# Kernel tuning notes

Measured on AMD Instinct MI355X. Metric: run time of the kernel, lower is better.

Reference implementation:

```python
import jax, jax.numpy as jnp
import numpy as np

# Architecture constants from Dense_test.__init__
N_HID = 200      # n
BRANCH = 8
IN_DIM = 120     # 40 * 3
N_OUT = 12
VTH = 1.0        # vth=1, dt=1 -> R*dt factor = 1

# Multi-gaussian surrogate-gradient spike (ActFun_adp from DH-SNN)
LENS, SCALE, HIGHT, GAMMA = 0.5, 6.0, 0.15, 0.5

@jax.custom_vjp
def spike_fn(v):
    return (v > 0).astype(v.dtype)

def _spike_fwd(v):
    return (v > 0).astype(v.dtype), v

def _gauss(x, mu, sigma):
    return jnp.exp(-((x - mu) ** 2) / (2.0 * sigma ** 2)) / (jnp.sqrt(2.0 * jnp.pi) * sigma)

def _spike_bwd(v, g):
    sg = (_gauss(v, 0.0, LENS) * (1.0 + HIGHT)
          - _gauss(v, LENS, SCALE * LENS) * HIGHT
          - _gauss(v, -LENS, SCALE * LENS) * HIGHT)
    return (g * sg * GAMMA,)

spike_fn.defvjp(_spike_fwd, _spike_bwd)


def make_branch_mask(rng, in_features, out_dim, branch):
    # Each output neuron's dendritic branches connect to disjoint random
    # subsets of (input + recurrent) lines.
    k = in_features // branch
    mask = np.zeros((out_dim * branch, in_features), np.float32)
    for i in range(out_dim):
        seq = rng.permutation(in_features)
        for j in range(branch):
            mask[i * branch + j, seq[j * k:(j + 1) * k]] = 1.0
    return jnp.asarray(mask)


def setup_inputs() -> dict:
    rng = np.random.default_rng(0)
    key = jax.random.key(0)
    ks = jax.random.split(key, 16)
    B, T = 1024, 101
    d = {"x": jax.random.normal(ks[0], (B, 3, T, 40), jnp.float32)}
    in_feats = [IN_DIM + N_HID, N_HID + N_HID, N_HID + N_HID]
    for li, in_f in enumerate(in_feats, start=1):
        mask = make_branch_mask(rng, in_f, N_HID, BRANCH)
        W = jax.random.normal(ks[li], (N_HID * BRANCH, in_f), jnp.float32) / np.sqrt(in_f)
        d[f"W{li}"] = W * mask   # mask is applied multiplicatively to dense weights
        d[f"b{li}"] = jnp.zeros((N_HID * BRANCH,), jnp.float32)
        d[f"tau_m{li}"] = jax.random.uniform(ks[li + 4], (N_HID,), jnp.float32, 0.0, 4.0)
        d[f"tau_n{li}"] = jax.random.uniform(ks[li + 8], (N_HID, BRANCH), jnp.float32, 0.0, 4.0)
    d["W4"] = jax.random.normal(ks[12], (N_OUT, N_HID), jnp.float32) / np.sqrt(N_HID)
    d["b4"] = jnp.zeros((N_OUT,), jnp.float32)
    d["tau_m4"] = jax.random.uniform(ks[13], (N_OUT,), jnp.float32, 0.0, 4.0)
    return d


def _forward(x, W1, b1, tau_m1, tau_n1, W2, b2, tau_m2, tau_n2,
             W3, b3, tau_m3, tau_n3, W4, b4, tau_m4):
    B, C, T, F = x.shape
    xs = jnp.transpose(x, (2, 0, 1, 3)).reshape(T, B, C * F)  # [T, B, 120]

    def dense_step(inp, spike, d, mem, W, b, tau_m, tau_n):
        k = jnp.concatenate([inp, spike], axis=1)              # recurrent concat
        ff = (k @ W.T + b).reshape(B, N_HID, BRANCH)
        beta = jax.nn.sigmoid(tau_n)                           # [N_HID, BRANCH]
        d = beta * d + (1.0 - beta) * ff                       # dendritic current
        alpha = jax.nn.sigmoid(tau_m)
        mem = (mem - VTH * spike) * alpha + (1.0 - alpha) * d.sum(-1)
        spike = spike_fn(mem - VTH)
        return spike, d, mem

    z = lambda *s: jnp.zeros(s, x.dtype)
    init = (z(B, N_HID), z(B, N_HID, BRANCH), z(B, N_HID),
            z(B, N_HID), z(B, N_HID, BRANCH), z(B, N_HID),
            z(B, N_HID), z(B, N_HID, BRANCH), z(B, N_HID),
            z(B, N_OUT), z(B, N_OUT))
    alpha4 = jax.nn.sigmoid(tau_m4)

    def step(carry, xt):
        s1, d1, m1, s2, d2, m2, s3, d3, m3, m4, acc = carry
        s1, d1, m1 = dense_step(xt, s1, d1, m1, W1, b1, tau_m1, tau_n1)
        s2, d2, m2 = dense_step(s1, s2, d2, m2, W2, b2, tau_m2, tau_n2)
        s3, d3, m3 = dense_step(s2, s3, d3, m3, W3, b3, tau_m3, tau_n3)
        m4 = m4 * alpha4 + (1.0 - alpha4) * (s3 @ W4.T + b4)   # leaky readout
        acc = acc + m4
        return (s1, d1, m1, s2, d2, m2, s3, d3, m3, m4, acc), None

    carry, _ = jax.lax.scan(step, init, xs)
    acc = carry[-1]
    return jax.nn.log_softmax(acc / T, axis=1)


def reference(x, W1, b1, tau_m1, tau_n1, W2, b2, tau_m2, tau_n2,
              W3, b3, tau_m3, tau_n3, W4, b4, tau_m4):
    return _forward(x, W1, b1, tau_m1, tau_n1, W2, b2, tau_m2, tau_n2,
                    W3, b3, tau_m3, tau_n3, W4, b4, tau_m4)
```

## Files before the change

### kernel.cpp

```cpp
#include <hip/hip_runtime.h>
#include <stdint.h>

#define T_STEPS 101
#define ROWS 1600
#define NTHR 1024
#define NBLK 256
#define NP1 20
#define NP23 25
#define PO2 (NP1 * ROWS)
#define PO3 (PO2 + NP23 * ROWS)
#define NPTOT (PO3 + NP23 * ROWS)

#define W2_OFF 0
#define C2_OFF (NPTOT * 8)
#define BB_OFF (C2_OFF + NPTOT * 4)
#define SA_OFF (BB_OFF + 3 * ROWS * 8)

__device__ __forceinline__ float sigmoidf(float v) { return 1.0f / (1.0f + expf(-v)); }

__global__ void prep_kernel(const float* __restrict__ W1, const float* __restrict__ W2,
                            const float* __restrict__ W3,
                            const float* __restrict__ b1, const float* __restrict__ tn1,
                            const float* __restrict__ tm1,
                            const float* __restrict__ b2, const float* __restrict__ tn2,
                            const float* __restrict__ tm2,
                            const float* __restrict__ b3, const float* __restrict__ tn3,
                            const float* __restrict__ tm3,
                            uint8_t* __restrict__ ws) {
  int gid = blockIdx.x * blockDim.x + threadIdx.x;
  if (gid >= 3 * ROWS) return;
  int l = gid / ROWS, r = gid - l * ROWS;
  const float *W, *bb, *tn, *tm; int in_f, knz, np, poff, scale;
  if (l == 0)      { W = W1; bb = b1; tn = tn1; tm = tm1; in_f = 320; knz = 40; np = NP1;  poff = 0;   scale = 16; }
  else if (l == 1) { W = W2; bb = b2; tn = tn2; tm = tm2; in_f = 400; knz = 50; np = NP23; poff = PO2; scale = 4; }
  else             { W = W3; bb = b3; tn = tn3; tm = tm3; in_f = 400; knz = 50; np = NP23; poff = PO3; scale = 4; }
  float2* w2 = (float2*)(ws + W2_OFF) + poff;
  uint32_t* c2 = (uint32_t*)(ws + C2_OFF) + poff;
  float wl[52]; uint32_t cl[52];
  int cnt = 0;
  for (int col = 0; col < in_f; ++col) {
    float w = W[(size_t)r * in_f + col];
    if (w != 0.0f && cnt < knz) { wl[cnt] = w; cl[cnt] = (uint32_t)(col * scale); ++cnt; }
  }
  for (; cnt < 2 * np; ++cnt) { wl[cnt] = 0.0f; cl[cnt] = 0u; }
  for (int p = 0; p < np; ++p) {
    w2[p * ROWS + r] = make_float2(wl[2 * p], wl[2 * p + 1]);
    c2[p * ROWS + r] = cl[2 * p] | (cl[2 * p + 1] << 16);
  }
  ((float2*)(ws + BB_OFF))[l * ROWS + r] = make_float2(sigmoidf(tn[r]), bb[r]);
  if (r < 200) ((float*)(ws + SA_OFF))[l * 200 + r] = sigmoidf(tm[r]);
}

template<int NP, bool F32>
__device__ __forceinline__ void slot_compute(
    int tid, int r,
    const float2* __restrict__ w2, const uint32_t* __restrict__ c2,
    const uint8_t* __restrict__ ktab,
    const float2* __restrict__ bbL, const float* __restrict__ saL,
    float (&dreg)[4], uint8_t (*s_l)[4], float (*mem_l)[4])
{
  const float2 bb = bbL[r];
  const float bt = bb.x;
  float a0 = bb.y, a1 = bb.y, a2 = bb.y, a3 = bb.y;
  const float2* wp = w2 + r;
  const uint32_t* cp = c2 + r;
#pragma unroll 5
  for (int p = 0; p < NP; ++p) {
    const float2 w = wp[(size_t)p * ROWS];
    const uint32_t c = cp[(size_t)p * ROWS];
    if constexpr (F32) {
      { const float4 kv = *reinterpret_cast<const float4*>(ktab + (c & 0xffffu));
        a0 = fmaf(w.x, kv.x, a0); a1 = fmaf(w.x, kv.y, a1);
        a2 = fmaf(w.x, kv.z, a2); a3 = fmaf(w.x, kv.w, a3); }
      { const float4 kv = *reinterpret_cast<const float4*>(ktab + (c >> 16));
        a0 = fmaf(w.y, kv.x, a0); a1 = fmaf(w.y, kv.y, a1);
        a2 = fmaf(w.y, kv.z, a2); a3 = fmaf(w.y, kv.w, a3); }
    } else {
      { const uint32_t q = *reinterpret_cast<const uint32_t*>(ktab + (c & 0xffffu));
        a0 = fmaf(w.x, (float)(q & 0xffu), a0);
        a1 = fmaf(w.x, (float)((q >> 8) & 0xffu), a1);
        a2 = fmaf(w.x, (float)((q >> 16) & 0xffu), a2);
        a3 = fmaf(w.x, (float)(q >> 24), a3); }
      { const uint32_t q = *reinterpret_cast<const uint32_t*>(ktab + (c >> 16));
        a0 = fmaf(w.y, (float)(q & 0xffu), a0);
        a1 = fmaf(w.y, (float)((q >> 8) & 0xffu), a1);
        a2 = fmaf(w.y, (float)((q >> 16) & 0xffu), a2);
        a3 = fmaf(w.y, (float)(q >> 24), a3); }
    }
  }
  const float ob = 1.0f - bt;
  float d0 = fmaf(bt, dreg[0], ob * a0);
  float d1 = fmaf(bt, dreg[1], ob * a1);
  float d2 = fmaf(bt, dreg[2], ob * a2);
  float d3 = fmaf(bt, dreg[3], ob * a3);
  dreg[0] = d0; dreg[1] = d1; dreg[2] = d2; dreg[3] = d3;
  d0 += __shfl_xor(d0, 1); d0 += __shfl_xor(d0, 2); d0 += __shfl_xor(d0, 4);
  d1 += __shfl_xor(d1, 1); d1 += __shfl_xor(d1, 2); d1 += __shfl_xor(d1, 4);
  d2 += __shfl_xor(d2, 1); d2 += __shfl_xor(d2, 2); d2 += __shfl_xor(d2, 4);
  d3 += __shfl_xor(d3, 1); d3 += __shfl_xor(d3, 2); d3 += __shfl_xor(d3, 4);
  if ((tid & 7) == 0) {
    const int n = r >> 3;
    const float al = saL[n], oa = 1.0f - al;
    float4 mv = *reinterpret_cast<float4*>(&mem_l[n][0]);
    const uint32_t so = *reinterpret_cast<uint32_t*>(&s_l[n][0]);
    const float m0 = fmaf(mv.x - (float)(so & 0xffu),         al, oa * d0);
    const float m1 = fmaf(mv.y - (float)((so >> 8) & 0xffu),  al, oa * d1);
    const float m2 = fmaf(mv.z - (float)((so >> 16) & 0xffu), al, oa * d2);
    const float m3 = fmaf(mv.w - (float)(so >> 24),           al, oa * d3);
    *reinterpret_cast<float4*>(&mem_l[n][0]) = make_float4(m0, m1, m2, m3);
    const uint32_t sn = (m0 > 1.0f ? 1u : 0u) | (m1 > 1.0f ? 0x100u : 0u)
                      | (m2 > 1.0f ? 0x10000u : 0u) | (m3 > 1.0f ? 0x1000000u : 0u);
    *reinterpret_cast<uint32_t*>(&s_l[n][0]) = sn;
  }
}

__global__ void __launch_bounds__(NTHR)
snn_main(const float* __restrict__ x,
         const float* __restrict__ W4, const float* __restrict__ b4,
         const float* __restrict__ tm4,
         const float2* __restrict__ w2G, const uint32_t* __restrict__ c2G,
         const float2* __restrict__ bbG, const float* __restrict__ saG,
         float* __restrict__ out)
{
  __shared__ __align__(16) float4   k1f[320];
  __shared__ __align__(4)  uint8_t  k23[400][4];
  __shared__ __align__(4)  uint8_t  s_lds[3][200][4];
  __shared__ __align__(16) float    mem_lds[3][200][4];
  __shared__ float  w4_lds[12][201];
  __shared__ float2 bbL[3 * ROWS];
  __shared__ float  saL[3 * 200];

  const int tid = threadIdx.x;
  const int bg  = blockIdx.x;

  for (int idx = tid; idx < 600; idx += NTHR) {
    reinterpret_cast<uint32_t*>(&s_lds[0][0][0])[idx] = 0u;
    reinterpret_cast<float4*>(&mem_lds[0][0][0])[idx] = make_float4(0.f, 0.f, 0.f, 0.f);
  }
  for (int idx = tid; idx < 12 * 200; idx += NTHR)
    w4_lds[idx / 200][idx % 200] = W4[idx];
  for (int idx = tid; idx < 3 * ROWS; idx += NTHR) bbL[idx] = bbG[idx];
  for (int idx = tid; idx < 3 * 200; idx += NTHR) saL[idx] = saG[idx];

  float d[3][2][4];
#pragma unroll
  for (int l = 0; l < 3; ++l)
#pragma unroll
    for (int i = 0; i < 2; ++i)
#pragma unroll
      for (int b = 0; b < 4; ++b) d[l][i][b] = 0.0f;

  const int r1 = tid + 576;
  float m4_reg = 0.0f, m4_acc = 0.0f, a4 = 0.0f, b4r = 0.0f;
  if (tid < 192) { const int o = (tid >> 2) >> 2; a4 = sigmoidf(tm4[o]); b4r = b4[o]; }
  __syncthreads();

  const uint8_t* k1b = reinterpret_cast<const uint8_t*>(&k1f[0]);
  const uint8_t* k2b = reinterpret_cast<const uint8_t*>(&k23[0][0]);

  for (int t = 0; t < T_STEPS; ++t) {
    if (tid < 480) {
      const int bat = tid / 120, cf = tid - bat * 120;
      const int c = cf / 40, f = cf - c * 40;
      reinterpret_cast<float*>(&k1f[cf])[bat] =
          x[(((size_t)(bg * 4 + bat) * 3 + c) * T_STEPS + t) * 40 + f];
    }
    if (tid < 200) {
      const uint32_t so = *reinterpret_cast<const uint32_t*>(&s_lds[0][tid][0]);
      k1f[120 + tid] = make_float4((float)(so & 0xffu), (float)((so >> 8) & 0xffu),
                                   (float)((so >> 16) & 0xffu), (float)(so >> 24));
    }
    __syncthreads();
    slot_compute<NP1, true>(tid, tid, w2G, c2G, k1b, bbL, saL,
                            d[0][0], s_lds[0], mem_lds[0]);
    if (tid >= 448)
      slot_compute<NP1, true>(tid, r1, w2G, c2G, k1b, bbL, saL,
                              d[0][1], s_lds[0], mem_lds[0]);
    __syncthreads();
    if (tid < 200)
      reinterpret_cast<uint32_t*>(&k23[0][0])[tid] =
          reinterpret_cast<const uint32_t*>(&s_lds[0][0][0])[tid];
    else if (tid < 400)
      reinterpret_cast<uint32_t*>(&k23[0][0])[tid] =
          reinterpret_cast<const uint32_t*>(&s_lds[1][0][0])[tid - 200];
    __syncthreads();
    slot_compute<NP23, false>(tid, tid, w2G + PO2, c2G + PO2, k2b, bbL + ROWS, saL + 200,
                              d[1][0], s_lds[1], mem_lds[1]);
    if (tid >= 448)
      slot_compute<NP23, false>(tid, r1, w2G + PO2, c2G + PO2, k2b, bbL + ROWS, saL + 200,
                                d[1][1], s_lds[1], mem_lds[1]);
    __syncthreads();
    if (tid < 200)
      reinterpret_cast<uint32_t*>(&k23[0][0])[tid] =
          reinterpret_cast<const uint32_t*>(&s_lds[1][0][0])[tid];
    else if (tid < 400)
      reinterpret_cast<uint32_t*>(&k23[0][0])[tid] =
          reinterpret_cast<const uint32_t*>(&s_lds[2][0][0])[tid - 200];
    __syncthreads();
    slot_compute<NP23, false>(tid, tid, w2G + PO3, c2G + PO3, k2b, bbL + 2 * ROWS, saL + 400,
                              d[2][0], s_lds[2], mem_lds[2]);
    if (tid >= 448)
      slot_compute<NP23, false>(tid, r1, w2G + PO3, c2G + PO3, k2b, bbL + 2 * ROWS, saL + 400,
                                d[2][1], s_lds[2], mem_lds[2]);
    __syncthreads();
    if (tid < 192) {
      const int sub = tid & 3, pair = tid >> 2, o = pair >> 2, bat = pair & 3;
      float part = 0.0f;
#pragma unroll 10
      for (int m = 0; m < 50; ++m) {
        const int n = 4 * m + sub;
        part = fmaf(w4_lds[o][n], (float)s_lds[2][n][bat], part);
      }
      part += __shfl_xor(part, 1);
      part += __shfl_xor(part, 2);
      const float dot = b4r + part;
      m4_reg = a4 * m4_reg + (1.0f - a4) * dot;
      m4_acc += m4_reg;
    }
  }

  __syncthreads();
  if (tid < 192 && (tid & 3) == 0) {
    const int pair = tid >> 2, o = pair >> 2, bat = pair & 3;
    reinterpret_cast<float*>(&k1f[o])[bat] = m4_acc * (1.0f / (float)T_STEPS);
  }
  __syncthreads();
  if (tid < 4) {
    const int bat = tid;
    float v[12], mx = -1e30f;
#pragma unroll
    for (int o = 0; o < 12; ++o) {
      v[o] = reinterpret_cast<float*>(&k1f[o])[bat];
      mx = fmaxf(mx, v[o]);
    }
    float s = 0.0f;
#pragma unroll
    for (int o = 0; o < 12; ++o) s += expf(v[o] - mx);
    const float ls = logf(s);
#pragma unroll
    for (int o = 0; o < 12; ++o)
      out[((size_t)(bg * 4 + bat)) * 12 + o] = v[o] - mx - ls;
  }
}

extern "C" void kernel_launch(void* const* d_in, const int* in_sizes, int n_in,
                              void* d_out, int out_size, void* d_ws, size_t ws_size,
                              hipStream_t stream) {
  (void)in_sizes; (void)n_in; (void)out_size; (void)ws_size;
  const float* x   = (const float*)d_in[0];
  const float* W1  = (const float*)d_in[1];
  const float* b1  = (const float*)d_in[2];
  const float* tm1 = (const float*)d_in[3];
  const float* tn1 = (const float*)d_in[4];
  const float* W2  = (const float*)d_in[5];
  const float* b2  = (const float*)d_in[6];
  const float* tm2 = (const float*)d_in[7];
  const float* tn2 = (const float*)d_in[8];
  const float* W3  = (const float*)d_in[9];
  const float* b3  = (const float*)d_in[10];
  const float* tm3 = (const float*)d_in[11];
  const float* tn3 = (const float*)d_in[12];
  const float* W4  = (const float*)d_in[13];
  const float* b4  = (const float*)d_in[14];
  const float* tm4 = (const float*)d_in[15];

  uint8_t* ws = (uint8_t*)d_ws;
  const float2*   w2G = (const float2*)(ws + W2_OFF);
  const uint32_t* c2G = (const uint32_t*)(ws + C2_OFF);
  const float2*   bbG = (const float2*)(ws + BB_OFF);
  const float*    saG = (const float*)(ws + SA_OFF);

  prep_kernel<<<dim3(19), dim3(256), 0, stream>>>(
      W1, W2, W3, b1, tn1, tm1, b2, tn2, tm2, b3, tn3, tm3, ws);
  snn_main<<<dim3(NBLK), dim3(NTHR), 0, stream>>>(
      x, W4, b4, tm4, w2G, c2G, bbG, saG, (float*)d_out);
}
```

Measured before the change: 3.188 ms.

## Double-buffer spike tables and prefetch inputs to cut per-step barriers

Spike outputs are written directly into double-buffered gather tables for the next layer and the next timestep, which removes the separate copy phases. This cuts the barriers per timestep from seven to three. The input x for step t+1 is prefetched by otherwise idle threads during layer 1, and the readout for step t-1 is overlapped with layer-1 compute, with a final readout after the loop. LDS use goes up and index bookkeeping gets more complex, and the readout's o/bat mapping is changed at the same time.

```diff
diff --git a/kernel.cpp b/kernel.cpp
--- a/kernel.cpp
+++ b/kernel.cpp
@@ -51,13 +51,14 @@
   if (r < 200) ((float*)(ws + SA_OFF))[l * 200 + r] = sigmoidf(tm[r]);
 }
 
-template<int NP, bool F32>
+template<int NP, bool F32, bool WA, bool WB, bool WK1>
 __device__ __forceinline__ void slot_compute(
     int tid, int r,
     const float2* __restrict__ w2, const uint32_t* __restrict__ c2,
     const uint8_t* __restrict__ ktab,
     const float2* __restrict__ bbL, const float* __restrict__ saL,
-    float (&dreg)[4], uint8_t (*s_l)[4], float (*mem_l)[4])
+    float (&dreg)[4], uint8_t (*s_l)[4], float (*mem_l)[4],
+    uint8_t (*spA)[4], uint8_t (*spB)[4], float4* k1n)
 {
   const float2 bb = bbL[r];
   const float bt = bb.x;
@@ -111,6 +112,11 @@
     const uint32_t sn = (m0 > 1.0f ? 1u : 0u) | (m1 > 1.0f ? 0x100u : 0u)
                       | (m2 > 1.0f ? 0x10000u : 0u) | (m3 > 1.0f ? 0x1000000u : 0u);
     *reinterpret_cast<uint32_t*>(&s_l[n][0]) = sn;
+    if constexpr (WA) *reinterpret_cast<uint32_t*>(&spA[n][0]) = sn;
+    if constexpr (WB) *reinterpret_cast<uint32_t*>(&spB[n][0]) = sn;
+    if constexpr (WK1)
+      k1n[120 + n] = make_float4(m0 > 1.0f ? 1.0f : 0.0f, m1 > 1.0f ? 1.0f : 0.0f,
+                                 m2 > 1.0f ? 1.0f : 0.0f, m3 > 1.0f ? 1.0f : 0.0f);
   }
 }
 
@@ -122,13 +128,15 @@
          const float2* __restrict__ bbG, const float* __restrict__ saG,
          float* __restrict__ out)
 {
-  __shared__ __align__(16) float4   k1f[320];
-  __shared__ __align__(4)  uint8_t  k23[400][4];
+  __shared__ __align__(16) float4   k1f[2][320];
+  __shared__ __align__(4)  uint8_t  k2tab[2][400][4];
+  __shared__ __align__(4)  uint8_t  k3tab[2][400][4];
   __shared__ __align__(4)  uint8_t  s_lds[3][200][4];
   __shared__ __align__(16) float    mem_lds[3][200][4];
   __shared__ float  w4_lds[12][201];
   __shared__ float2 bbL[3 * ROWS];
   __shared__ float  saL[3 * 200];
+  __shared__ float  smx[12][4];
 
   const int tid = threadIdx.x;
   const int bg  = blockIdx.x;
@@ -137,10 +145,22 @@
     reinterpret_cast<uint32_t*>(&s_lds[0][0][0])[idx] = 0u;
     reinterpret_cast<float4*>(&mem_lds[0][0][0])[idx] = make_float4(0.f, 0.f, 0.f, 0.f);
   }
+  for (int idx = tid; idx < 800; idx += NTHR) {
+    reinterpret_cast<uint32_t*>(&k2tab[0][0][0])[idx] = 0u;
+    reinterpret_cast<uint32_t*>(&k3tab[0][0][0])[idx] = 0u;
+  }
+  for (int idx = tid; idx < 200; idx += NTHR)
+    k1f[0][120 + idx] = make_float4(0.f, 0.f, 0.f, 0.f);
   for (int idx = tid; idx < 12 * 200; idx += NTHR)
     w4_lds[idx / 200][idx % 200] = W4[idx];
   for (int idx = tid; idx < 3 * ROWS; idx += NTHR) bbL[idx] = bbG[idx];
   for (int idx = tid; idx < 3 * 200; idx += NTHR) saL[idx] = saG[idx];
+  if (tid < 480) {
+    const int bat = tid / 120, cf = tid - bat * 120;
+    const int c = cf / 40, f = cf - c * 40;
+    reinterpret_cast<float*>(&k1f[0][cf])[bat] =
+        x[(((size_t)(bg * 4 + bat) * 3 + c) * T_STEPS) * 40 + f];
+  }
 
   float d[3][2][4];
 #pragma unroll
@@ -152,64 +172,55 @@
 
   const int r1 = tid + 576;
   float m4_reg = 0.0f, m4_acc = 0.0f, a4 = 0.0f, b4r = 0.0f;
-  if (tid < 192) { const int o = (tid >> 2) >> 2; a4 = sigmoidf(tm4[o]); b4r = b4[o]; }
+  if (tid < 192) { const int o = tid >> 4; a4 = sigmoidf(tm4[o]); b4r = b4[o]; }
+  const float* xpA = nullptr; const float* xpB = nullptr;
+  int dofA = 0, dofB = 0;
+  if (tid >= 192 && tid < 448) {
+    const int q0 = tid - 192;
+    { const int bat = q0 / 120, cf = q0 - bat * 120;
+      const int c = cf / 40, f = cf - c * 40;
+      xpA = x + (((size_t)(bg * 4 + bat) * 3 + c) * T_STEPS) * 40 + f;
+      dofA = cf * 4 + bat; }
+    const int q1 = q0 + 256;
+    if (q1 < 480) {
+      const int bat = q1 / 120, cf = q1 - bat * 120;
+      const int c = cf / 40, f = cf - c * 40;
+      xpB = x + (((size_t)(bg * 4 + bat) * 3 + c) * T_STEPS) * 40 + f;
+      dofB = cf * 4 + bat;
+    }
+  }
   __syncthreads();
 
-  const uint8_t* k1b = reinterpret_cast<const uint8_t*>(&k1f[0]);
-  const uint8_t* k2b = reinterpret_cast<const uint8_t*>(&k23[0][0]);
-
   for (int t = 0; t < T_STEPS; ++t) {
-    if (tid < 480) {
-      const int bat = tid / 120, cf = tid - bat * 120;
-      const int c = cf / 40, f = cf - c * 40;
-      reinterpret_cast<float*>(&k1f[cf])[bat] =
-          x[(((size_t)(bg * 4 + bat) * 3 + c) * T_STEPS + t) * 40 + f];
-    }
-    if (tid < 200) {
-      const uint32_t so = *reinterpret_cast<const uint32_t*>(&s_lds[0][tid][0]);
-      k1f[120 + tid] = make_float4((float)(so & 0xffu), (float)((so >> 8) & 0xffu),
-                                   (float)((so >> 16) & 0xffu), (float)(so >> 24));
-    }
-    __syncthreads();
-    slot_compute<NP1, true>(tid, tid, w2G, c2G, k1b, bbL, saL,
-                            d[0][0], s_lds[0], mem_lds[0]);
-    if (tid >= 448)
-      slot_compute<NP1, true>(tid, r1, w2G, c2G, k1b, bbL, saL,
-                              d[0][1], s_lds[0], mem_lds[0]);
-    __syncthreads();
-    if (tid < 200)
-      reinterpret_cast<uint32_t*>(&k23[0][0])[tid] =
-          reinterpret_cast<const uint32_t*>(&s_lds[0][0][0])[tid];
-    else if (tid < 400)
-      reinterpret_cast<uint32_t*>(&k23[0][0])[tid] =
-          reinterpret_cast<const uint32_t*>(&s_lds[1][0][0])[tid - 200];
-    __syncthreads();
-    slot_compute<NP23, false>(tid, tid, w2G + PO2, c2G + PO2, k2b, bbL + ROWS, saL + 200,
-                              d[1][0], s_lds[1], mem_lds[1]);
-    if (tid >= 448)
-      slot_compute<NP23, false>(tid, r1, w2G + PO2, c2G + PO2, k2b, bbL + ROWS, saL + 200,
-                                d[1][1], s_lds[1], mem_lds[1]);
-    __syncthreads();
-    if (tid < 200)
-      reinterpret_cast<uint32_t*>(&k23[0][0])[tid] =
-          reinterpret_cast<const uint32_t*>(&s_lds[1][0][0])[tid];
-    else if (tid < 400)
-      reinterpret_cast<uint32_t*>(&k23[0][0])[tid] =
-          reinterpret_cast<const uint32_t*>(&s_lds[2][0][0])[tid - 200];
-    __syncthreads();
-    slot_compute<NP23, false>(tid, tid, w2G + PO3, c2G + PO3, k2b, bbL + 2 * ROWS, saL + 400,
-                              d[2][0], s_lds[2], mem_lds[2]);
-    if (tid >= 448)
-      slot_compute<NP23, false>(tid, r1, w2G + PO3, c2G + PO3, k2b, bbL + 2 * ROWS, saL + 400,
-                                d[2][1], s_lds[2], mem_lds[2]);
-    __syncthreads();
-    if (tid < 192) {
-      const int sub = tid & 3, pair = tid >> 2, o = pair >> 2, bat = pair & 3;
+    const int cur = t & 1, nxt = cur ^ 1;
+    const uint8_t* k1b = reinterpret_cast<const uint8_t*>(&k1f[cur][0]);
+    const uint8_t* k2b = reinterpret_cast<const uint8_t*>(&k2tab[cur][0][0]);
+    const uint8_t* k3b = reinterpret_cast<const uint8_t*>(&k3tab[cur][0][0]);
+    float xv0 = 0.f, xv1 = 0.f;
+    const bool doX = (tid >= 192 && tid < 448) && (t + 1 < T_STEPS);
+    if (doX) {
+      xv0 = xpA[(t + 1) * 40];
+      if (xpB) xv1 = xpB[(t + 1) * 40];
+    }
+    slot_compute<NP1, true, true, false, true>(
+        tid, tid, w2G, c2G, k1b, bbL, saL, d[0][0], s_lds[0], mem_lds[0],
+        k2tab[cur], k2tab[cur], k1f[nxt]);
+    if (tid >= 448) {
+      slot_compute<NP1, true, true, false, true>(
+          tid, r1, w2G, c2G, k1b, bbL, saL, d[0][1], s_lds[0], mem_lds[0],
+          k2tab[cur], k2tab[cur], k1f[nxt]);
+    } else if (tid >= 192) {
+      if (doX) {
+        reinterpret_cast<float*>(&k1f[nxt][0])[dofA] = xv0;
+        if (xpB) reinterpret_cast<float*>(&k1f[nxt][0])[dofB] = xv1;
+      }
+    } else if (t > 0) {
+      const int sub = tid & 3, pair = tid >> 2, o = pair >> 4, bat = pair & 3;
       float part = 0.0f;
 #pragma unroll 10
       for (int m = 0; m < 50; ++m) {
         const int n = 4 * m + sub;
-        part = fmaf(w4_lds[o][n], (float)s_lds[2][n][bat], part);
+        part = fmaf(w4_lds[(tid >> 4)][n], (float)s_lds[2][n][(tid >> 2) & 3], part);
       }
       part += __shfl_xor(part, 1);
       part += __shfl_xor(part, 2);
@@ -217,22 +228,47 @@
       m4_reg = a4 * m4_reg + (1.0f - a4) * dot;
       m4_acc += m4_reg;
     }
-  }
-
-  __syncthreads();
-  if (tid < 192 && (tid & 3) == 0) {
-    const int pair = tid >> 2, o = pair >> 2, bat = pair & 3;
-    reinterpret_cast<float*>(&k1f[o])[bat] = m4_acc * (1.0f / (float)T_STEPS);
+    __syncthreads();
+    slot_compute<NP23, false, true, true, false>(
+        tid, tid, w2G + PO2, c2G + PO2, k2b, bbL + ROWS, saL + 200,
+        d[1][0], s_lds[1], mem_lds[1], k3tab[cur], k2tab[nxt] + 200, nullptr);
+    if (tid >= 448)
+      slot_compute<NP23, false, true, true, false>(
+          tid, r1, w2G + PO2, c2G + PO2, k2b, bbL + ROWS, saL + 200,
+          d[1][1], s_lds[1], mem_lds[1], k3tab[cur], k2tab[nxt] + 200, nullptr);
+    __syncthreads();
+    slot_compute<NP23, false, false, true, false>(
+        tid, tid, w2G + PO3, c2G + PO3, k3b, bbL + 2 * ROWS, saL + 400,
+        d[2][0], s_lds[2], mem_lds[2], k3tab[cur], k3tab[nxt] + 200, nullptr);
+    if (tid >= 448)
+      slot_compute<NP23, false, false, true, false>(
+          tid, r1, w2G + PO3, c2G + PO3, k3b, bbL + 2 * ROWS, saL + 400,
+          d[2][1], s_lds[2], mem_lds[2], k3tab[cur], k3tab[nxt] + 200, nullptr);
+    __syncthreads();
+  }
+
+  if (tid < 192) {
+    const int sub = tid & 3;
+    float part = 0.0f;
+#pragma unroll 10
+    for (int m = 0; m < 50; ++m) {
+      const int n = 4 * m + sub;
+      part = fmaf(w4_lds[(tid >> 4)][n], (float)s_lds[2][n][(tid >> 2) & 3], part);
+    }
+    part += __shfl_xor(part, 1);
+    part += __shfl_xor(part, 2);
+    const float dot = b4r + part;
+    m4_reg = a4 * m4_reg + (1.0f - a4) * dot;
+    m4_acc += m4_reg;
+    if ((tid & 3) == 0)
+      smx[tid >> 4][(tid >> 2) & 3] = m4_acc * (1.0f / (float)T_STEPS);
   }
   __syncthreads();
   if (tid < 4) {
     const int bat = tid;
     float v[12], mx = -1e30f;
 #pragma unroll
-    for (int o = 0; o < 12; ++o) {
-      v[o] = reinterpret_cast<float*>(&k1f[o])[bat];
-      mx = fmaxf(mx, v[o]);
-    }
+    for (int o = 0; o < 12; ++o) { v[o] = smx[o][bat]; mx = fmaxf(mx, v[o]); }
     float s = 0.0f;
 #pragma unroll
     for (int o = 0; o < 12; ++o) s += expf(v[o] - mx);
```

New measurement: 3.147 ms. About the same (-1.3%).
